# Kernel tuning notes

Measured on AMD Instinct MI355X. Metric: run time of the kernel, lower is better.

## Reference

```python
import jax, jax.numpy as jnp
import numpy as np

EPS = 1e-5  # torch BatchNorm default eps
B, C, T, NOUT, NCLS = 4096, 32, 512, 16, 4


def setup_inputs() -> dict:
    key = jax.random.key(0)
    ks = jax.random.split(key, 12)
    s = lambda k, shape: jax.random.normal(k, shape, jnp.float32) * 0.05
    return {
        "de": jax.random.normal(ks[0], (B, C, T), jnp.float32),
        "adj": jax.random.normal(ks[1], (B, C, C), jnp.float32),  # unused by forward (module recomputes corr)
        "dw_w": s(ks[2], (C, 1, 3)),      # depthwise Conv1d weight [C,1,3]
        "dw_b": s(ks[3], (C,)),
        "pw_w": s(ks[4], (C, C)),          # pointwise 1x1 conv [out,in]
        "pw_b": s(ks[5], (C,)),
        "bn1_g": jnp.ones((C,), jnp.float32),
        "bn1_b": jnp.zeros((C,), jnp.float32),
        "gc_w": s(ks[6], (T, NOUT)),       # GraphConvolution weight
        "fc_w": s(ks[7], (C * NOUT, C)),   # fc62 Linear(512,32)
        "fc_b": s(ks[8], (C,)),
        "bn2_g": jnp.ones((C,), jnp.float32),
        "bn2_b": jnp.zeros((C,), jnp.float32),
        "cls_w": s(ks[9], (C, NCLS)),      # fcclass Linear(32,4)
        "cls_b": s(ks[10], (NCLS,)),
    }


def reference(de, adj, dw_w, dw_b, pw_w, pw_b, bn1_g, bn1_b, gc_w,
              fc_w, fc_b, bn2_g, bn2_b, cls_w, cls_b):
    # --- SeparableConv2d (really 1d): depthwise k=3 -> pointwise 1x1 -> BN -> relu ---
    x = jax.lax.conv_general_dilated(
        de, dw_w, window_strides=(1,), padding=[(1, 1)],
        dimension_numbers=("NCH", "OIH", "NCH"),
        feature_group_count=de.shape[1]) + dw_b[None, :, None]
    x = jnp.einsum("oc,bct->bot", pw_w, x) + pw_b[None, :, None]
    m = x.mean((0, 2), keepdims=True)
    v = x.var((0, 2), keepdims=True)  # biased, as BN normalization uses
    x = (x - m) / jnp.sqrt(v + EPS) * bn1_g[None, :, None] + bn1_b[None, :, None]
    x = jax.nn.relu(x)                       # [B, C, T]

    # --- batched Pearson corrcoef over the time axis (vectorizes the per-sample loop) ---
    xt = x.transpose(0, 2, 1)                # [B, T, C]
    Tn = xt.shape[1]
    f = (Tn - 1) / Tn
    xc = xt - xt.mean(1, keepdims=True)
    num = jnp.einsum("btn,btm->bnm", xc, xc) / Tn   # biased covariance
    var = xt.var(1, ddof=1)                         # torch var default unbiased
    den = jnp.sqrt(var[:, :, None] * var[:, None, :]) * f
    cor = num / den                          # [B, C, C]

    # --- Chebyshev graph convolution (single K term, adj = cor) + relu ---
    g = jnp.einsum("bnm,bmt->bnt", cor, x)   # message passing over channel graph
    g = jax.nn.relu(jnp.einsum("bnt,to->bno", g, gc_w))  # [B, C, 16]

    # --- fc62: Linear -> BN1d -> (dropout: identity) -> sigmoid ---
    h = g.reshape(g.shape[0], -1) @ fc_w + fc_b          # [B, 32]
    m2 = h.mean(0)
    v2 = h.var(0)
    h = (h - m2) / jnp.sqrt(v2 + EPS) * bn2_g + bn2_b
    h = jax.nn.sigmoid(h)

    return h @ cls_w + cls_b                 # [B, 4]
```

## Files before the change

### kernel.cpp

```cpp
#include <hip/hip_runtime.h>
#include <math.h>

#define BB 4096
#define CC 32
#define TT 512
#define NOUTC 16
#define EPSF 1e-5f
#define XS 520


typedef __attribute__((ext_vector_type(16))) float f32x16;
typedef __attribute__((ext_vector_type(4)))  float f32x4;
typedef __attribute__((ext_vector_type(8)))  short short8;
typedef __attribute__((ext_vector_type(8)))  _Float16 half8;
typedef __attribute__((ext_vector_type(4)))  unsigned int u32x4;
typedef __attribute__((ext_vector_type(4)))  float vf4;
typedef vf4 __attribute__((aligned(4))) vf4u;

__device__ __forceinline__ unsigned short f2b(float f) {
  unsigned int u = __builtin_bit_cast(unsigned int, f);
  return (unsigned short)((u + 0x7FFFu + ((u >> 16) & 1u)) >> 16);
}
__device__ __forceinline__ float blo(unsigned int u) {
  return __builtin_bit_cast(float, u << 16);
}
__device__ __forceinline__ float bhi(unsigned int u) {
  return __builtin_bit_cast(float, u & 0xFFFF0000u);
}
__device__ __forceinline__ unsigned int pk2(float a, float b) {
  return (unsigned int)f2b(a) | ((unsigned int)f2b(b) << 16);
}
__device__ __forceinline__ unsigned short h16(float f) {
  _Float16 h = (_Float16)f;
  return __builtin_bit_cast(unsigned short, h);
}
__device__ __forceinline__ unsigned int h2pk(float a, float b) {
  return (unsigned int)h16(a) | ((unsigned int)h16(b) << 16);
}

__device__ __forceinline__ void conv_cols(const float* __restrict__ deb,
    const float* __restrict__ dw, const float* __restrict__ db_,
    int tid, float* x1A, float* x1B) {
  int t0 = tid * 2;
  int off = (tid == 0) ? 0 : ((tid == 255) ? t0 - 2 : t0 - 1);
#pragma unroll
  for (int c = 0; c < CC; c++) {
    vf4u v = *reinterpret_cast<const vf4u*>(deb + c * TT + off);
    float vm1 = (tid == 0) ? 0.f : ((tid == 255) ? v.y : v.x);
    float v0  = (tid == 0) ? v.x : ((tid == 255) ? v.z : v.y);
    float vp1 = (tid == 0) ? v.y : ((tid == 255) ? v.w : v.z);
    float vp2 = (tid == 0) ? v.z : ((tid == 255) ? 0.f : v.w);
    float w0 = dw[c * 3], w1 = dw[c * 3 + 1], w2 = dw[c * 3 + 2], bc = db_[c];
    x1A[c] = fmaf(w0, vm1, fmaf(w1, v0, fmaf(w2, vp1, bc)));
    x1B[c] = fmaf(w0, v0, fmaf(w1, vp1, fmaf(w2, vp2, bc)));
  }
}

__device__ __forceinline__ void stage_row_f16(unsigned short* lds1, int row, const float* x) {
#pragma unroll
  for (int cb = 0; cb < 4; cb++) {
    u32x4 v;
#pragma unroll
    for (int k = 0; k < 4; k++) v[k] = h2pk(x[cb * 8 + 2 * k], x[cb * 8 + 2 * k + 1]);
    *(u32x4*)&lds1[row * 40 + cb * 8] = v;
  }
}

__global__ __launch_bounds__(256, 3) void k1_stats(const float* __restrict__ de,
    const float* __restrict__ dw, const float* __restrict__ db_,
    const float* __restrict__ pw, const float* __restrict__ pwb,
    float* __restrict__ part, unsigned int* __restrict__ x2h, int useWs) {
  __shared__ __align__(16) unsigned short lds1[19712];
  const int XFo = 0, X2Bo = 10240, PWFo = 18688;

  int tid = threadIdx.x, b = blockIdx.x;
  int lane = tid & 63, w = tid >> 6;
  int m31 = lane & 31, kh = lane >> 5;
  int hw = tid >> 5, l32 = tid & 31;

  const float* deb = de + (size_t)b * CC * TT;
  float x1A[CC], x1B[CC];
  conv_cols(deb, dw, db_, tid, x1A, x1B);

  for (int i = tid; i < CC * CC; i += 256) lds1[PWFo + i] = h16(pw[i]);
  __syncthreads();

  half8 ah[2];
#pragma unroll
  for (int s = 0; s < 2; s++)
    ah[s] = *(const half8*)&lds1[PWFo + m31 * 32 + s * 16 + kh * 8];
  float pbv[16];
#pragma unroll
  for (int r = 0; r < 16; r++) pbv[r] = pwb[(r & 3) + 8 * (r >> 2) + 4 * kh];

  unsigned int* xw = x2h + (size_t)b * (CC * 256);
  float sAcc[4] = {0.f, 0.f, 0.f, 0.f}, qAcc[4] = {0.f, 0.f, 0.f, 0.f};

#pragma unroll
  for (int h = 0; h < 2; h++) {
    if ((tid >> 7) == h) {
      int lr = 2 * (tid & 127);
      stage_row_f16(lds1, lr, x1A);
      stage_row_f16(lds1, lr + 1, x1B);
    }
    __syncthreads();

#pragma unroll
    for (int i = 0; i < 2; i++) {
      int wt = w * 2 + i;
      f32x16 acc;
#pragma unroll
      for (int r = 0; r < 16; r++) acc[r] = 0.f;
      int rowb = wt * 32 + m31;
#pragma unroll
      for (int s = 0; s < 2; s++) {
        half8 bh = *(const half8*)&lds1[XFo + rowb * 40 + s * 16 + kh * 8];
        acc = __builtin_amdgcn_mfma_f32_32x32x16_f16(ah[s], bh, acc, 0, 0, 0);
      }
      int tloc = wt * 32 + m31;
#pragma unroll
      for (int pr = 0; pr < 8; pr++) {
        int o0 = ((2 * pr) & 3) + 8 * (pr >> 1) + 4 * kh;
        unsigned int p = pk2(acc[2 * pr] + pbv[2 * pr], acc[2 * pr + 1] + pbv[2 * pr + 1]);
        lds1[X2Bo + o0 * 264 + tloc] = (unsigned short)(p & 0xFFFFu);
        lds1[X2Bo + (o0 + 1) * 264 + tloc] = (unsigned short)(p >> 16);
      }
    }
    __syncthreads();

#pragma unroll
    for (int it = 0; it < 4; it++) {
      int o = it * 8 + hw;
      u32x4 v = *(const u32x4*)&lds1[X2Bo + o * 264 + l32 * 8];
      float s = 0.f, q = 0.f;
#pragma unroll
      for (int k = 0; k < 4; k++) {
        float a = blo(v[k]), c2 = bhi(v[k]);
        s += a + c2;
        q = fmaf(a, a, fmaf(c2, c2, q));
      }
#pragma unroll
      for (int d = 1; d < 32; d <<= 1) { s += __shfl_xor(s, d); q += __shfl_xor(q, d); }
      sAcc[it] += s; qAcc[it] += q;
      if (useWs) *(u32x4*)(xw + (size_t)h * 4096 + o * 128 + l32 * 4) = v;
    }
  }

  if (l32 == 0) {
#pragma unroll
    for (int it = 0; it < 4; it++) {
      int o = it * 8 + hw;
      part[(size_t)o * BB + b] = sAcc[it];
      part[(size_t)(32 + o) * BB + b] = qAcc[it];
    }
  }
}

__global__ void k2_bn1(const float* __restrict__ part, const float* __restrict__ g,
                       const float* __restrict__ bta, float* __restrict__ ws,
                       const float* __restrict__ gcw, unsigned short* __restrict__ gcf) {
  __shared__ float redS[256], redQ[256];
  int o = blockIdx.x, tid = threadIdx.x;
  {
    int i = o * 256 + tid;
    int e = i & 7, ln = (i >> 3) & 63, j = (i >> 9) & 7, w2 = i >> 12;
    int q = ln >> 4, n16 = ln & 15;
    int t = w2 * 256 + q * 8 + j * 32 + e;
    gcf[i] = f2b(gcw[t * 16 + n16]);
  }
  const float* ps = part + (size_t)o * BB;
  const float* pq = part + (size_t)(CC + o) * BB;
  float s = 0, q = 0;
  for (int i = tid; i < BB; i += 256) { s += ps[i]; q += pq[i]; }
  redS[tid] = s; redQ[tid] = q;
  __syncthreads();
  for (int k = 128; k > 0; k >>= 1) {
    if (tid < k) { redS[tid] += redS[tid + k]; redQ[tid] += redQ[tid + k]; }
    __syncthreads();
  }
  if (tid == 0) {
    float N = (float)BB * (float)TT;
    float mean = redS[0] / N;
    float var = redQ[0] / N - mean * mean;
    float sc = g[o] / sqrtf(var + EPSF);
    ws[o] = sc;
    ws[32 + o] = bta[o] - mean * sc;
  }
}

__global__ __launch_bounds__(256, 3) void k3_main(const float* __restrict__ de,
    const float* __restrict__ dw, const float* __restrict__ db_,
    const float* __restrict__ pw, const float* __restrict__ pwb,
    const float* __restrict__ ws, const unsigned short* __restrict__ gcf,
    const float* __restrict__ fcw, const float* __restrict__ fcb,
    float* __restrict__ hT, const unsigned int* __restrict__ x2h, int useWs) {
  __shared__ __align__(16) unsigned short x_s[CC * XS];
  __shared__ float gramP[2][CC * CC];
  __shared__ float zP[2][CC * NOUTC];
  __shared__ float red16[CC * 8];
  __shared__ float mu_s[CC], inv_s[CC];

  int tid = threadIdx.x, b = blockIdx.x;
  int w = tid >> 6, lane = tid & 63;
  int t0 = tid * 2;

  if (useWs) {
    const unsigned int* xr = x2h + (size_t)b * (CC * 256);
    int base = (tid >> 7) * 4096 + (tid & 127);
#pragma unroll
    for (int o = 0; o < CC; o++) {
      unsigned int u = xr[base + o * 128];
      float sc = ws[o], sh = ws[32 + o];
      unsigned short hA = f2b(fmaxf(fmaf(blo(u), sc, sh), 0.f));
      unsigned short hB = f2b(fmaxf(fmaf(bhi(u), sc, sh), 0.f));
      *(unsigned int*)(&x_s[o * XS + t0]) = (unsigned int)hA | ((unsigned int)hB << 16);
    }
  } else {
    const float* deb = de + (size_t)b * CC * TT;
    float x1A[CC], x1B[CC];
    conv_cols(deb, dw, db_, tid, x1A, x1B);
#pragma unroll
    for (int o = 0; o < CC; o++) {
      float aA = pwb[o], aB = pwb[o];
#pragma unroll
      for (int c = 0; c < CC; c++) { float pv = pw[o * CC + c]; aA = fmaf(pv, x1A[c], aA); aB = fmaf(pv, x1B[c], aB); }
      float sc = ws[o], sh = ws[32 + o];
      unsigned short hA = f2b(fmaxf(fmaf(aA, sc, sh), 0.f));
      unsigned short hB = f2b(fmaxf(fmaf(aB, sc, sh), 0.f));
      *(unsigned int*)(&x_s[o * XS + t0]) = (unsigned int)hA | ((unsigned int)hB << 16);
    }
  }
  __syncthreads();

  {
    int c = tid >> 3, j = tid & 7;
    float s = 0.f;
#pragma unroll
    for (int it = 0; it < 8; it++) {
      u32x4 u = *reinterpret_cast<const u32x4*>(&x_s[c * XS + j * 64 + it * 8]);
#pragma unroll
      for (int k = 0; k < 4; k++) s += blo(u[k]) + bhi(u[k]);
    }
    red16[c * 8 + j] = s;
  }

  if (w < 2) {
    int m = lane & 31, kh = lane >> 5;
    f32x16 acc;
#pragma unroll
    for (int r = 0; r < 16; r++) acc[r] = 0.f;
    int kbase = w * 256 + kh * 8;
#pragma unroll
    for (int kk = 0; kk < 256; kk += 16) {
      short8 a = *(const short8*)(&x_s[m * XS + kbase + kk]);
      acc = __builtin_amdgcn_mfma_f32_32x32x16_bf16(a, a, acc, 0, 0, 0);
    }
#pragma unroll
    for (int r = 0; r < 16; r++) {
      int row = (r & 3) + 8 * (r >> 2) + 4 * kh;
      gramP[w][row * CC + m] = acc[r];
    }
  } else {
    int w2 = w - 2;
    int n16 = lane & 15, q = lane >> 4;
    f32x4 ac0, ac1;
#pragma unroll
    for (int r = 0; r < 4; r++) { ac0[r] = 0.f; ac1[r] = 0.f; }
    const unsigned short* gf = gcf + w2 * 4096;
    short8 bfr[8];
#pragma unroll
    for (int j = 0; j < 8; j++) bfr[j] = *(const short8*)(gf + (j * 64 + lane) * 8);
    int kbase = w2 * 256 + q * 8;
#pragma unroll
    for (int j = 0; j < 8; j++) {
      int kk = j * 32;
      short8 af0 = *(const short8*)(&x_s[n16 * XS + kbase + kk]);
      short8 af1 = *(const short8*)(&x_s[(16 + n16) * XS + kbase + kk]);
      ac0 = __builtin_amdgcn_mfma_f32_16x16x32_bf16(af0, bfr[j], ac0, 0, 0, 0);
      ac1 = __builtin_amdgcn_mfma_f32_16x16x32_bf16(af1, bfr[j], ac1, 0, 0, 0);
    }
#pragma unroll
    for (int r = 0; r < 4; r++) {
      int row = q * 4 + r;
      zP[w2][row * NOUTC + n16] = ac0[r];
      zP[w2][(16 + row) * NOUTC + n16] = ac1[r];
    }
  }
  __syncthreads();
  if (tid < CC) {
    float s = 0.f;
#pragma unroll
    for (int j = 0; j < 8; j++) s += red16[tid * 8 + j];
    mu_s[tid] = s;
  }
  __syncthreads();
  float* gram0 = gramP[0];
  float* Zi = zP[0];
  float* g2 = zP[1];
  for (int i = tid; i < CC * CC; i += 256) {
    int n = i >> 5, m = i & 31;
    gram0[i] = gram0[i] + gramP[1][i] - mu_s[n] * mu_s[m] * (1.f / (float)TT);
  }
  for (int i = tid; i < CC * NOUTC; i += 256) Zi[i] = zP[0][i] + zP[1][i];
  __syncthreads();
  if (tid < CC) inv_s[tid] = rsqrtf(gram0[tid * 32 + tid]);
  __syncthreads();
  for (int i = tid; i < CC * NOUTC; i += 256) {
    int n = i >> 4, o = i & 15;
    float s = 0.f;
#pragma unroll
    for (int m = 0; m < CC; m++) s = fmaf(gram0[n * 32 + m] * inv_s[m], Zi[m * NOUTC + o], s);
    g2[i] = fmaxf(s * inv_s[n], 0.f);
  }
  __syncthreads();
  float* red2 = gramP[1];
  {
    int j = tid & 31, ch = tid >> 5;
    float p = 0.f;
#pragma unroll
    for (int ii = 0; ii < 64; ii++) {
      int i = ch * 64 + ii;
      p = fmaf(g2[i], fcw[i * CC + j], p);
    }
    red2[j * 9 + ch] = p;
  }
  __syncthreads();
  if (tid < CC) {
    float h = fcb[tid];
#pragma unroll
    for (int ch = 0; ch < 8; ch++) h += red2[tid * 9 + ch];
    hT[(size_t)tid * BB + b] = h;
  }
}

__global__ void k4_bn2(const float* __restrict__ hT, const float* __restrict__ g,
                       const float* __restrict__ bta, float* __restrict__ ws) {
  __shared__ float redS[256], redQ[256];
  int j = blockIdx.x, tid = threadIdx.x;
  const float* row = hT + (size_t)j * BB;
  float s = 0, q = 0;
  for (int i = tid; i < BB; i += 256) { float v = row[i]; s += v; q = fmaf(v, v, q); }
  redS[tid] = s; redQ[tid] = q;
  __syncthreads();
  for (int k = 128; k > 0; k >>= 1) {
    if (tid < k) { redS[tid] += redS[tid + k]; redQ[tid] += redQ[tid + k]; }
    __syncthreads();
  }
  if (tid == 0) {
    float N = (float)BB;
    float mean = redS[0] / N;
    float var = redQ[0] / N - mean * mean;
    float sc = g[j] / sqrtf(var + EPSF);
    ws[64 + j] = sc;
    ws[96 + j] = bta[j] - mean * sc;
  }
}

__global__ void k5_out(const float* __restrict__ hT, const float* __restrict__ ws,
                       const float* __restrict__ clsw, const float* __restrict__ clsb,
                       float* __restrict__ out) {
  __shared__ float hs[CC * 257];
  int b0 = blockIdx.x * 256, tid = threadIdx.x;
  for (int i = tid; i < CC * 256; i += 256) {
    int j = i >> 8, bb = i & 255;
    float v = fmaf(hT[(size_t)j * BB + b0 + bb], ws[64 + j], ws[96 + j]);
    hs[j * 257 + bb] = 1.f / (1.f + expf(-v));
  }
  __syncthreads();
  float o0 = clsb[0], o1 = clsb[1], o2 = clsb[2], o3 = clsb[3];
#pragma unroll
  for (int j = 0; j < CC; j++) {
    float h = hs[j * 257 + tid];
    o0 = fmaf(h, clsw[j * 4 + 0], o0);
    o1 = fmaf(h, clsw[j * 4 + 1], o1);
    o2 = fmaf(h, clsw[j * 4 + 2], o2);
    o3 = fmaf(h, clsw[j * 4 + 3], o3);
  }
  float4* out4 = reinterpret_cast<float4*>(out);
  out4[b0 + tid] = make_float4(o0, o1, o2, o3);
}

extern "C" void kernel_launch(void* const* d_in, const int* in_sizes, int n_in,
                              void* d_out, int out_size, void* d_ws, size_t ws_size,
                              hipStream_t stream) {
  const float* de   = (const float*)d_in[0];
  const float* dw   = (const float*)d_in[2];
  const float* db_  = (const float*)d_in[3];
  const float* pw   = (const float*)d_in[4];
  const float* pwb  = (const float*)d_in[5];
  const float* bn1g = (const float*)d_in[6];
  const float* bn1b = (const float*)d_in[7];
  const float* gcw  = (const float*)d_in[8];
  const float* fcw  = (const float*)d_in[9];
  const float* fcb  = (const float*)d_in[10];
  const float* bn2g = (const float*)d_in[11];
  const float* bn2b = (const float*)d_in[12];
  const float* clsw = (const float*)d_in[13];
  const float* clsb = (const float*)d_in[14];

  float* ws = (float*)d_ws;
  unsigned short* gcf = (unsigned short*)(ws + 128);
  float* hT   = ws + 4224;
  float* part = ws + 135296;
  unsigned int* x2h = (unsigned int*)(ws + 397440);
  float* out  = (float*)d_out;

  size_t need = ((size_t)397440 + 33554432ull) * 4ull;
  int useWs = (ws_size >= need) ? 1 : 0;

  k1_stats<<<BB, 256, 0, stream>>>(de, dw, db_, pw, pwb, part, x2h, useWs);
  k2_bn1<<<CC, 256, 0, stream>>>(part, bn1g, bn1b, ws, gcw, gcf);
  k3_main<<<BB, 256, 0, stream>>>(de, dw, db_, pw, pwb, ws, gcf, fcw, fcb, hT, x2h, useWs);
  k4_bn2<<<CC, 256, 0, stream>>>(hT, bn2g, bn2b, ws);
  k5_out<<<BB / 256, 256, 0, stream>>>(hT, ws, clsw, clsb, out);
}
```

Measured before the change: 487.0 us.

## Fold depthwise conv into MFMA, write MFMA-layout workspace, atomic BN1 stats, drop k2

k1 now folds the depthwise 3-tap conv into the pointwise GEMM by precomputing three combined weight matrices, so it runs three shifted f16 MFMAs over a raw-input tile staged in LDS. The conv bias becomes a folded pointwise bias. Per-channel sums and sums of squares are kept in registers and reduced with shuffles plus global atomics, which removes the LDS transpose, the partials array and the k2 reduction kernel. The bf16 intermediate is written straight from MFMA register order, and k3 re-maps it and computes the BN1 scale and shift itself. The costs are a memset, float atomic ordering nondeterminism, and scattered 16-bit LDS writes in k3.

```diff
diff --git a/kernel.cpp b/kernel.cpp
--- a/kernel.cpp
+++ b/kernel.cpp
@@ -14,8 +14,11 @@
 typedef __attribute__((ext_vector_type(8)))  short short8;
 typedef __attribute__((ext_vector_type(8)))  _Float16 half8;
 typedef __attribute__((ext_vector_type(4)))  unsigned int u32x4;
+typedef __attribute__((ext_vector_type(2)))  unsigned int u32x2;
+typedef __attribute__((ext_vector_type(2)))  float vf2;
 typedef __attribute__((ext_vector_type(4)))  float vf4;
 typedef vf4 __attribute__((aligned(4))) vf4u;
+typedef vf2 __attribute__((aligned(4))) vf2u;
 
 __device__ __forceinline__ unsigned short f2b(float f) {
   unsigned int u = __builtin_bit_cast(unsigned int, f);
@@ -56,55 +59,82 @@
   }
 }
 
-__device__ __forceinline__ void stage_row_f16(unsigned short* lds1, int row, const float* x) {
-#pragma unroll
-  for (int cb = 0; cb < 4; cb++) {
-    u32x4 v;
-#pragma unroll
-    for (int k = 0; k < 4; k++) v[k] = h2pk(x[cb * 8 + 2 * k], x[cb * 8 + 2 * k + 1]);
-    *(u32x4*)&lds1[row * 40 + cb * 8] = v;
-  }
-}
-
-__global__ __launch_bounds__(256, 3) void k1_stats(const float* __restrict__ de,
+__global__ __launch_bounds__(256, 4) void k1_stats(const float* __restrict__ de,
     const float* __restrict__ dw, const float* __restrict__ db_,
     const float* __restrict__ pw, const float* __restrict__ pwb,
-    float* __restrict__ part, unsigned int* __restrict__ x2h, int useWs) {
-  __shared__ __align__(16) unsigned short lds1[19712];
-  const int XFo = 0, X2Bo = 10240, PWFo = 18688;
+    const float* __restrict__ gcw,
+    float* __restrict__ wsv, unsigned short* __restrict__ gcf,
+    unsigned int* __restrict__ x2h, int useWs) {
+  __shared__ __align__(16) unsigned short ldsX[13392];
+  __shared__ float pbe_s[CC];
+  __shared__ float sqb[4][64];
+  const int XFo = 0, A3o = 10320;
 
   int tid = threadIdx.x, b = blockIdx.x;
   int lane = tid & 63, w = tid >> 6;
   int m31 = lane & 31, kh = lane >> 5;
-  int hw = tid >> 5, l32 = tid & 31;
+  int p = tid >> 7, rp = tid & 127;
+
+  if (b == 0) {
+    for (int i = tid; i < TT * NOUTC; i += 256) {
+      int e = i & 7, ln = (i >> 3) & 63, j = (i >> 9) & 7, w2 = i >> 12;
+      int q = ln >> 4, n16 = ln & 15;
+      int t = w2 * 256 + q * 8 + j * 32 + e;
+      gcf[i] = f2b(gcw[t * 16 + n16]);
+    }
+  }
+
+  for (int i = tid; i < 3 * CC * CC; i += 256) {
+    int k = i >> 10, rem = i & 1023, o = rem >> 5, c = rem & 31;
+    ldsX[A3o + i] = h16(pw[o * CC + c] * dw[c * 3 + k]);
+  }
+  if (tid < CC) {
+    float s = pwb[tid];
+#pragma unroll
+    for (int c = 0; c < CC; c++) s = fmaf(pw[tid * CC + c], db_[c], s);
+    pbe_s[tid] = s;
+  }
 
   const float* deb = de + (size_t)b * CC * TT;
-  float x1A[CC], x1B[CC];
-  conv_cols(deb, dw, db_, tid, x1A, x1B);
-
-  for (int i = tid; i < CC * CC; i += 256) lds1[PWFo + i] = h16(pw[i]);
-  __syncthreads();
-
-  half8 ah[2];
-#pragma unroll
-  for (int s = 0; s < 2; s++)
-    ah[s] = *(const half8*)&lds1[PWFo + m31 * 32 + s * 16 + kh * 8];
+  unsigned int* xw = x2h + (size_t)b * (CC * 256);
+
+  float sA[16], qA[16];
+#pragma unroll
+  for (int r = 0; r < 16; r++) { sA[r] = 0.f; qA[r] = 0.f; }
   float pbv[16];
-#pragma unroll
-  for (int r = 0; r < 16; r++) pbv[r] = pwb[(r & 3) + 8 * (r >> 2) + 4 * kh];
-
-  unsigned int* xw = x2h + (size_t)b * (CC * 256);
-  float sAcc[4] = {0.f, 0.f, 0.f, 0.f}, qAcc[4] = {0.f, 0.f, 0.f, 0.f};
 
 #pragma unroll
   for (int h = 0; h < 2; h++) {
-    if ((tid >> 7) == h) {
-      int lr = 2 * (tid & 127);
-      stage_row_f16(lds1, lr, x1A);
-      stage_row_f16(lds1, lr + 1, x1B);
+    if (h > 0) __syncthreads();
+    {
+      int t0 = h * 256 + 2 * rp - 1;
+      int r0 = 2 * rp;
+      int tl = (t0 < 0) ? 0 : t0;
+#pragma unroll
+      for (int cc = 0; cc < 16; cc += 2) {
+        int c = 16 * p + cc;
+        vf2 va = *(const vf2u*)(deb + c * TT + tl);
+        vf2 vb = *(const vf2u*)(deb + (c + 1) * TT + tl);
+        if (t0 < 0) { va.y = va.x; va.x = 0.f; vb.y = vb.x; vb.x = 0.f; }
+        *(unsigned int*)&ldsX[XFo + r0 * 40 + c] = h2pk(va.x, vb.x);
+        *(unsigned int*)&ldsX[XFo + (r0 + 1) * 40 + c] = h2pk(va.y, vb.y);
+      }
+      if (rp >= 126) {
+        int r2 = 256 + (rp - 126);
+        int t2 = h * 256 + r2 - 1;
+#pragma unroll
+        for (int cc = 0; cc < 16; cc++) {
+          int c = 16 * p + cc;
+          float v = (t2 < TT) ? deb[c * TT + t2] : 0.f;
+          ldsX[XFo + r2 * 40 + c] = h16(v);
+        }
+      }
     }
     __syncthreads();
-
+    if (h == 0) {
+#pragma unroll
+      for (int r = 0; r < 16; r++) pbv[r] = pbe_s[(r & 3) + 8 * (r >> 2) + 4 * kh];
+    }
 #pragma unroll
     for (int i = 0; i < 2; i++) {
       int wt = w * 2 + i;
@@ -113,85 +143,62 @@
       for (int r = 0; r < 16; r++) acc[r] = 0.f;
       int rowb = wt * 32 + m31;
 #pragma unroll
-      for (int s = 0; s < 2; s++) {
-        half8 bh = *(const half8*)&lds1[XFo + rowb * 40 + s * 16 + kh * 8];
-        acc = __builtin_amdgcn_mfma_f32_32x32x16_f16(ah[s], bh, acc, 0, 0, 0);
+      for (int k = 0; k < 3; k++) {
+#pragma unroll
+        for (int s = 0; s < 2; s++) {
+          half8 af = *(const half8*)&ldsX[A3o + k * 1024 + m31 * 32 + s * 16 + kh * 8];
+          half8 bf = *(const half8*)&ldsX[XFo + (rowb + k) * 40 + s * 16 + kh * 8];
+          acc = __builtin_amdgcn_mfma_f32_32x32x16_f16(af, bf, acc, 0, 0, 0);
+        }
       }
-      int tloc = wt * 32 + m31;
-#pragma unroll
-      for (int pr = 0; pr < 8; pr++) {
-        int o0 = ((2 * pr) & 3) + 8 * (pr >> 1) + 4 * kh;
-        unsigned int p = pk2(acc[2 * pr] + pbv[2 * pr], acc[2 * pr + 1] + pbv[2 * pr + 1]);
-        lds1[X2Bo + o0 * 264 + tloc] = (unsigned short)(p & 0xFFFFu);
-        lds1[X2Bo + (o0 + 1) * 264 + tloc] = (unsigned short)(p >> 16);
+#pragma unroll
+      for (int q4 = 0; q4 < 4; q4++) {
+        float v0 = acc[4 * q4 + 0] + pbv[4 * q4 + 0];
+        float v1 = acc[4 * q4 + 1] + pbv[4 * q4 + 1];
+        float v2 = acc[4 * q4 + 2] + pbv[4 * q4 + 2];
+        float v3 = acc[4 * q4 + 3] + pbv[4 * q4 + 3];
+        sA[4 * q4 + 0] += v0; qA[4 * q4 + 0] = fmaf(v0, v0, qA[4 * q4 + 0]);
+        sA[4 * q4 + 1] += v1; qA[4 * q4 + 1] = fmaf(v1, v1, qA[4 * q4 + 1]);
+        sA[4 * q4 + 2] += v2; qA[4 * q4 + 2] = fmaf(v2, v2, qA[4 * q4 + 2]);
+        sA[4 * q4 + 3] += v3; qA[4 * q4 + 3] = fmaf(v3, v3, qA[4 * q4 + 3]);
+        if (useWs) {
+          u32x2 pr2;
+          pr2[0] = pk2(v0, v1);
+          pr2[1] = pk2(v2, v3);
+          *(u32x2*)(xw + ((((size_t)h * 8 + wt) * 4 + q4) * 2 + kh) * 64 + m31 * 2) = pr2;
+        }
       }
     }
-    __syncthreads();
-
-#pragma unroll
-    for (int it = 0; it < 4; it++) {
-      int o = it * 8 + hw;
-      u32x4 v = *(const u32x4*)&lds1[X2Bo + o * 264 + l32 * 8];
-      float s = 0.f, q = 0.f;
-#pragma unroll
-      for (int k = 0; k < 4; k++) {
-        float a = blo(v[k]), c2 = bhi(v[k]);
-        s += a + c2;
-        q = fmaf(a, a, fmaf(c2, c2, q));
-      }
-#pragma unroll
-      for (int d = 1; d < 32; d <<= 1) { s += __shfl_xor(s, d); q += __shfl_xor(q, d); }
-      sAcc[it] += s; qAcc[it] += q;
-      if (useWs) *(u32x4*)(xw + (size_t)h * 4096 + o * 128 + l32 * 4) = v;
-    }
-  }
-
-  if (l32 == 0) {
-#pragma unroll
-    for (int it = 0; it < 4; it++) {
-      int o = it * 8 + hw;
-      part[(size_t)o * BB + b] = sAcc[it];
-      part[(size_t)(32 + o) * BB + b] = qAcc[it];
-    }
-  }
-}
-
-__global__ void k2_bn1(const float* __restrict__ part, const float* __restrict__ g,
-                       const float* __restrict__ bta, float* __restrict__ ws,
-                       const float* __restrict__ gcw, unsigned short* __restrict__ gcf) {
-  __shared__ float redS[256], redQ[256];
-  int o = blockIdx.x, tid = threadIdx.x;
-  {
-    int i = o * 256 + tid;
-    int e = i & 7, ln = (i >> 3) & 63, j = (i >> 9) & 7, w2 = i >> 12;
-    int q = ln >> 4, n16 = ln & 15;
-    int t = w2 * 256 + q * 8 + j * 32 + e;
-    gcf[i] = f2b(gcw[t * 16 + n16]);
-  }
-  const float* ps = part + (size_t)o * BB;
-  const float* pq = part + (size_t)(CC + o) * BB;
-  float s = 0, q = 0;
-  for (int i = tid; i < BB; i += 256) { s += ps[i]; q += pq[i]; }
-  redS[tid] = s; redQ[tid] = q;
-  __syncthreads();
-  for (int k = 128; k > 0; k >>= 1) {
-    if (tid < k) { redS[tid] += redS[tid + k]; redQ[tid] += redQ[tid + k]; }
-    __syncthreads();
-  }
-  if (tid == 0) {
-    float N = (float)BB * (float)TT;
-    float mean = redS[0] / N;
-    float var = redQ[0] / N - mean * mean;
-    float sc = g[o] / sqrtf(var + EPSF);
-    ws[o] = sc;
-    ws[32 + o] = bta[o] - mean * sc;
+  }
+
+#pragma unroll
+  for (int r = 0; r < 16; r++) {
+    float s = sA[r], q = qA[r];
+#pragma unroll
+    for (int d = 1; d < 32; d <<= 1) { s += __shfl_xor(s, d); q += __shfl_xor(q, d); }
+    sA[r] = s; qA[r] = q;
+  }
+  if (m31 == 0) {
+#pragma unroll
+    for (int r = 0; r < 16; r++) {
+      int o = (r & 3) + 8 * (r >> 2) + 4 * kh;
+      sqb[w][o * 2 + 0] = sA[r];
+      sqb[w][o * 2 + 1] = qA[r];
+    }
+  }
+  __syncthreads();
+  if (tid < 64) {
+    int o = tid >> 1, st = tid & 1;
+    float v = sqb[0][tid] + sqb[1][tid] + sqb[2][tid] + sqb[3][tid];
+    atomicAdd(&wsv[st * 32 + o], v);
   }
 }
 
 __global__ __launch_bounds__(256, 3) void k3_main(const float* __restrict__ de,
     const float* __restrict__ dw, const float* __restrict__ db_,
     const float* __restrict__ pw, const float* __restrict__ pwb,
-    const float* __restrict__ ws, const unsigned short* __restrict__ gcf,
+    const float* __restrict__ wsv, const float* __restrict__ bn1g,
+    const float* __restrict__ bn1b, const unsigned short* __restrict__ gcf,
     const float* __restrict__ fcw, const float* __restrict__ fcb,
     float* __restrict__ hT, const unsigned int* __restrict__ x2h, int useWs) {
   __shared__ __align__(16) unsigned short x_s[CC * XS];
@@ -199,21 +206,40 @@
   __shared__ float zP[2][CC * NOUTC];
   __shared__ float red16[CC * 8];
   __shared__ float mu_s[CC], inv_s[CC];
+  __shared__ float scsh[64];
 
   int tid = threadIdx.x, b = blockIdx.x;
   int w = tid >> 6, lane = tid & 63;
   int t0 = tid * 2;
 
+  if (tid < CC) {
+    float N = (float)BB * (float)TT;
+    float mean = wsv[tid] / N;
+    float var = wsv[32 + tid] / N - mean * mean;
+    float sc = bn1g[tid] / sqrtf(var + EPSF);
+    scsh[tid] = sc;
+    scsh[32 + tid] = bn1b[tid] - mean * sc;
+  }
+  __syncthreads();
+
   if (useWs) {
     const unsigned int* xr = x2h + (size_t)b * (CC * 256);
-    int base = (tid >> 7) * 4096 + (tid & 127);
-#pragma unroll
-    for (int o = 0; o < CC; o++) {
-      unsigned int u = xr[base + o * 128];
-      float sc = ws[o], sh = ws[32 + o];
-      unsigned short hA = f2b(fmaxf(fmaf(blo(u), sc, sh), 0.f));
-      unsigned short hB = f2b(fmaxf(fmaf(bhi(u), sc, sh), 0.f));
-      *(unsigned int*)(&x_s[o * XS + t0]) = (unsigned int)hA | ((unsigned int)hB << 16);
+#pragma unroll
+    for (int it = 0; it < 16; it++) {
+      int g = it * 256 + tid;
+      int m31g = g & 31, khg = (g >> 5) & 1, q4g = (g >> 6) & 3;
+      int wtg = (g >> 8) & 7, hg = (g >> 11) & 1;
+      u32x2 v = *(const u32x2*)(xr + (size_t)g * 2);
+      int ob = 8 * q4g + 4 * khg;
+      int t = hg * 256 + wtg * 32 + m31g;
+      float f0 = fmaxf(fmaf(blo(v[0]), scsh[ob + 0], scsh[32 + ob + 0]), 0.f);
+      float f1 = fmaxf(fmaf(bhi(v[0]), scsh[ob + 1], scsh[32 + ob + 1]), 0.f);
+      float f2 = fmaxf(fmaf(blo(v[1]), scsh[ob + 2], scsh[32 + ob + 2]), 0.f);
+      float f3 = fmaxf(fmaf(bhi(v[1]), scsh[ob + 3], scsh[32 + ob + 3]), 0.f);
+      x_s[(ob + 0) * XS + t] = f2b(f0);
+      x_s[(ob + 1) * XS + t] = f2b(f1);
+      x_s[(ob + 2) * XS + t] = f2b(f2);
+      x_s[(ob + 3) * XS + t] = f2b(f3);
     }
   } else {
     const float* deb = de + (size_t)b * CC * TT;
@@ -224,7 +250,7 @@
       float aA = pwb[o], aB = pwb[o];
 #pragma unroll
       for (int c = 0; c < CC; c++) { float pv = pw[o * CC + c]; aA = fmaf(pv, x1A[c], aA); aB = fmaf(pv, x1B[c], aB); }
-      float sc = ws[o], sh = ws[32 + o];
+      float sc = scsh[o], sh = scsh[32 + o];
       unsigned short hA = f2b(fmaxf(fmaf(aA, sc, sh), 0.f));
       unsigned short hB = f2b(fmaxf(fmaf(aB, sc, sh), 0.f));
       *(unsigned int*)(&x_s[o * XS + t0]) = (unsigned int)hA | ((unsigned int)hB << 16);
@@ -316,13 +342,13 @@
   float* red2 = gramP[1];
   {
     int j = tid & 31, ch = tid >> 5;
-    float p = 0.f;
+    float pacc = 0.f;
 #pragma unroll
     for (int ii = 0; ii < 64; ii++) {
       int i = ch * 64 + ii;
-      p = fmaf(g2[i], fcw[i * CC + j], p);
-    }
-    red2[j * 9 + ch] = p;
+      pacc = fmaf(g2[i], fcw[i * CC + j], pacc);
+    }
+    red2[j * 9 + ch] = pacc;
   }
   __syncthreads();
   if (tid < CC) {
@@ -401,16 +427,15 @@
   float* ws = (float*)d_ws;
   unsigned short* gcf = (unsigned short*)(ws + 128);
   float* hT   = ws + 4224;
-  float* part = ws + 135296;
   unsigned int* x2h = (unsigned int*)(ws + 397440);
   float* out  = (float*)d_out;
 
   size_t need = ((size_t)397440 + 33554432ull) * 4ull;
   int useWs = (ws_size >= need) ? 1 : 0;
 
-  k1_stats<<<BB, 256, 0, stream>>>(de, dw, db_, pw, pwb, part, x2h, useWs);
-  k2_bn1<<<CC, 256, 0, stream>>>(part, bn1g, bn1b, ws, gcw, gcf);
-  k3_main<<<BB, 256, 0, stream>>>(de, dw, db_, pw, pwb, ws, gcf, fcw, fcb, hT, x2h, useWs);
+  hipMemsetAsync(d_ws, 0, 256, stream);
+  k1_stats<<<BB, 256, 0, stream>>>(de, dw, db_, pw, pwb, gcw, ws, gcf, x2h, useWs);
+  k3_main<<<BB, 256, 0, stream>>>(de, dw, db_, pw, pwb, ws, bn1g, bn1b, gcf, fcw, fcb, hT, x2h, useWs);
   k4_bn2<<<CC, 256, 0, stream>>>(hT, bn2g, bn2b, ws);
   k5_out<<<BB / 256, 256, 0, stream>>>(hT, ws, clsw, clsb, out);
 }
```

Measured after the change: 524.7 us. 7.7% more time.
